# Kernel tuning notes

Measured on AMD Instinct MI355X. Metric: run time of the kernel, lower is better.

## Reference

```python
import jax, jax.numpy as jnp
import numpy as np

B, T, D_MODEL = 4, 4096, 512
HEADS, BUCKET_SIZE, N_HASHES = 8, 64, 4
DIM_HEAD = D_MODEL // HEADS  # 64
D_FFN = 2048
N_BUCKETS = T // BUCKET_SIZE  # 64
SELF_ATTN_VALUE = -5e4  # reformer TOKEN_SELF_ATTN_VALUE


def setup_inputs() -> dict:
    key = jax.random.key(0)
    ks = jax.random.split(key, 16)
    s = 0.02
    return {
        'x': jax.random.normal(ks[0], (B, T, D_MODEL), jnp.float32),
        'rotations': jax.random.normal(ks[1], (DIM_HEAD, N_HASHES, N_BUCKETS // 2), jnp.float32),
        'w_qk': jax.random.normal(ks[2], (D_MODEL, D_MODEL), jnp.float32) * s,
        'w_v': jax.random.normal(ks[3], (D_MODEL, D_MODEL), jnp.float32) * s,
        'w_out': jax.random.normal(ks[4], (D_MODEL, D_MODEL), jnp.float32) * s,
        'b_out': jnp.zeros((D_MODEL,), jnp.float32),
        'ln1_g': jnp.ones((D_MODEL,), jnp.float32),
        'ln1_b': jnp.zeros((D_MODEL,), jnp.float32),
        'w1': jax.random.normal(ks[5], (D_FFN, D_MODEL), jnp.float32) * s,
        'b1': jnp.zeros((D_FFN,), jnp.float32),
        'w2': jax.random.normal(ks[6], (D_MODEL, D_FFN), jnp.float32) * s,
        'b2': jnp.zeros((D_MODEL,), jnp.float32),
        'ln2_g': jnp.ones((D_MODEL,), jnp.float32),
        'ln2_b': jnp.zeros((D_MODEL,), jnp.float32),
    }


def layer_norm(x, g, b, eps=1e-6):
    m = x.mean(-1, keepdims=True)
    v = ((x - m) ** 2).mean(-1, keepdims=True)
    return (x - m) / jnp.sqrt(v + eps) * g + b


def look_one_back(x):
    # concat each chunk with the previous chunk (wrap-around), along in-chunk axis
    prev = jnp.roll(x, 1, axis=1)
    return jnp.concatenate([x, prev], axis=2)


def lsh_attention(qk, v, rotations):
    # qk, v: (bh, t, d) with shared-QK; rotations: (d, n_hashes, n_buckets//2)
    bh, t, d = qk.shape
    # --- hash: random rotations, argmax over [R, -R] ---
    rot = jnp.einsum('btf,fhi->bhti', qk, rotations)
    rot = jnp.concatenate([rot, -rot], axis=-1)        # (bh, H, t, n_buckets)
    buckets = jnp.argmax(rot, axis=-1)                 # (bh, H, t)
    buckets = buckets + (jnp.arange(N_HASHES) * N_BUCKETS)[None, :, None]
    buckets = buckets.reshape(bh, N_HASHES * t)
    # --- sort by (bucket, position) ---
    ticker = jnp.arange(N_HASHES * t)
    buckets_and_t = t * buckets + (ticker % t)[None, :]
    sticker = jnp.argsort(buckets_and_t, axis=-1)      # stable sort
    undo_sort = jnp.argsort(sticker, axis=-1)
    st = sticker % t                                   # original positions, sorted order
    sqk = jnp.take_along_axis(qk, st[..., None], axis=1)
    sv = jnp.take_along_axis(v, st[..., None], axis=1)
    # --- chunk: n_hashes*n_buckets chunks of bucket_size tokens ---
    n_chunks = N_HASHES * N_BUCKETS
    bq_t = st.reshape(bh, n_chunks, -1)
    bqk = sqk.reshape(bh, n_chunks, -1, d)
    bv = sv.reshape(bh, n_chunks, -1, d)
    bk = bqk / jnp.clip(jnp.linalg.norm(bqk, axis=-1, keepdims=True), 1e-6, None)
    bk = look_one_back(bk)
    bv = look_one_back(bv)
    bkv_t = look_one_back(bq_t)
    # --- local attention within chunk (+ previous chunk) ---
    dots = jnp.einsum('bcid,bcjd->bcij', bqk, bk) * (DIM_HEAD ** -0.5)
    self_mask = bq_t[..., None] == bkv_t[..., None, :]
    dots = jnp.where(self_mask, SELF_ATTN_VALUE, dots)
    logits = jax.nn.logsumexp(dots, axis=-1, keepdims=True)
    probs = jnp.exp(dots - logits)
    bo = jnp.einsum('bcij,bcjd->bcid', probs, bv)
    # --- unsort and combine hash rounds by softmax over round logits ---
    so = bo.reshape(bh, N_HASHES * t, d)
    slogits = logits.reshape(bh, N_HASHES * t)
    o = jnp.take_along_axis(so, undo_sort[..., None], axis=1).reshape(bh, N_HASHES, t, d)
    lg = jnp.take_along_axis(slogits, undo_sort, axis=1).reshape(bh, N_HASHES, t, 1)
    w = jnp.exp(lg - jax.nn.logsumexp(lg, axis=1, keepdims=True))
    return (o * w).sum(axis=1)                         # (bh, t, d)


def reference(x, rotations, w_qk, w_v, w_out, b_out, ln1_g, ln1_b, w1, b1, w2, b2, ln2_g, ln2_b):
    b, t, _ = x.shape
    qk = x @ w_qk.T
    v = x @ w_v.T

    def split_heads(u):
        return u.reshape(b, t, HEADS, DIM_HEAD).transpose(0, 2, 1, 3).reshape(b * HEADS, t, DIM_HEAD)

    attn = lsh_attention(split_heads(qk), split_heads(v), rotations)
    attn = attn.reshape(b, HEADS, t, DIM_HEAD).transpose(0, 2, 1, 3).reshape(b, t, D_MODEL)
    attn = attn @ w_out.T + b_out
    # residual + LN (dropout is identity at inference)
    h = layer_norm(attn + x, ln1_g, ln1_b)
    # position-wise FFN with its own residual + LN
    f = jax.nn.relu(h @ w1.T + b1) @ w2.T + b2
    return layer_norm(f + h, ln2_g, ln2_b)
```

## Files before the change

### kernel.cpp

```cpp
#include <hip/hip_runtime.h>
#include <stdint.h>

typedef unsigned short u16;
typedef __attribute__((ext_vector_type(4))) int   i32x4;
typedef __attribute__((ext_vector_type(4))) float f32x4;

__device__ __forceinline__ u16 f2bf(float x){
  unsigned int u = __float_as_uint(x);
  u += 0x7FFFu + ((u >> 16) & 1u);
  return (u16)(u >> 16);
}
__device__ __forceinline__ float bf2f(u16 h){
  return __uint_as_float(((unsigned int)h) << 16);
}
__device__ __forceinline__ f32x4 mfma16(i32x4 a, i32x4 b, f32x4 c){
  asm("v_mfma_f32_16x16x32_bf16 %0, %1, %2, %0" : "+v"(c) : "v"(a), "v"(b));
  return c;
}
__device__ __forceinline__ f32x4 acc_fence(f32x4 c){
  asm volatile("s_nop 7\ns_nop 7" : "+v"(c));
  return c;
}
__device__ __forceinline__ void gl_lds16(const void* g, void* l){
  unsigned long long ga = (unsigned long long)g;
  unsigned int la = (unsigned int)(unsigned long long)l;
  __builtin_amdgcn_global_load_lds((const __attribute__((address_space(1))) void*)ga,
                                   (__attribute__((address_space(3))) void*)la, 16, 0, 0);
}
__device__ __forceinline__ unsigned int f2mono(float v){
  unsigned int u = __float_as_uint(v);
  return u ^ ((unsigned int)((int)u >> 31) | 0x80000000u);
}
__device__ __forceinline__ float mono2f(unsigned int mu){
  unsigned int u = (mu & 0x80000000u) ? (mu ^ 0x80000000u) : ~mu;
  return __uint_as_float(u);
}
__device__ __forceinline__ unsigned long long shfl_xor_u64(unsigned long long x, int m){
  int lo = __shfl_xor((int)(unsigned int)(x & 0xFFFFFFFFull), m);
  int hi = __shfl_xor((int)(unsigned int)(x >> 32), m);
  return ((unsigned long long)(unsigned int)hi << 32) | (unsigned int)lo;
}

__global__ __launch_bounds__(256) void k_cvt(const float* __restrict__ in, u16* __restrict__ out, int n4){
  int i = blockIdx.x*256 + threadIdx.x;
  if (i >= n4) return;
  float4 v = ((const float4*)in)[i];
  ushort4 o; o.x=f2bf(v.x); o.y=f2bf(v.y); o.z=f2bf(v.z); o.w=f2bf(v.w);
  ((ushort4*)out)[i] = o;
}
__global__ __launch_bounds__(256) void k_split(const float* __restrict__ in, u16* __restrict__ hi, u16* __restrict__ lo, int n4){
  int i = blockIdx.x*256 + threadIdx.x;
  if (i >= n4) return;
  float4 v = ((const float4*)in)[i];
  ushort4 h, l;
  h.x=f2bf(v.x); l.x=f2bf(v.x - bf2f(h.x));
  h.y=f2bf(v.y); l.y=f2bf(v.y - bf2f(h.y));
  h.z=f2bf(v.z); l.z=f2bf(v.z - bf2f(h.z));
  h.w=f2bf(v.w); l.w=f2bf(v.w - bf2f(h.w));
  ((ushort4*)hi)[i]=h; ((ushort4*)lo)[i]=l;
}
__global__ __launch_bounds__(256) void k_rotT(const float* __restrict__ rot, u16* __restrict__ hi, u16* __restrict__ lo){
  int i = blockIdx.x*256 + threadIdx.x;
  if (i >= 8192) return;
  int d = i & 63, n = i >> 6;
  float v = rot[d*128 + n];
  u16 h = f2bf(v);
  hi[i] = h; lo[i] = f2bf(v - bf2f(h));
}

template<int MODE>
__global__ __launch_bounds__(256) void k_gemm(
    const u16* __restrict__ A0, const u16* __restrict__ A1,
    const u16* __restrict__ B0, const u16* __restrict__ B1,
    const float* __restrict__ bias,
    float* __restrict__ Cf, u16* __restrict__ Cb,
    int M, int N, int K, int nterms)
{
  const int tid = threadIdx.x;
  const int l = tid & 63, w = tid >> 6;
  const int lr = l & 15, lg = l >> 4;
  const int m0 = blockIdx.y * 128, n0 = blockIdx.x * 128;
  const int mbase = (w >> 1) * 64, nbase = (w & 1) * 64;

  __shared__ __align__(16) u16 As[128*64];
  __shared__ __align__(16) u16 Bs[128*64];

  f32x4 zero = {0.f,0.f,0.f,0.f};
  f32x4 acc[4][4];
  #pragma unroll
  for (int i=0;i<4;i++)
    #pragma unroll
    for (int j=0;j<4;j++) acc[i][j] = zero;

  const int row_s = tid >> 3;
  const int c16   = tid & 7;

  for (int term = 0; term < nterms; ++term){
    const u16* Ap = (term==2) ? A1 : A0;
    const u16* Bp = (term==1) ? B1 : B0;
    for (int k0 = 0; k0 < K; k0 += 64){
      #pragma unroll
      for (int q=0;q<4;q++){
        int ra = q*32 + row_s;
        int cs = c16 ^ (ra & 7);
        gl_lds16(Ap + (size_t)(m0 + ra)*K + k0 + cs*8, (char*)As + q*4096 + tid*16);
        gl_lds16(Bp + (size_t)(n0 + ra)*K + k0 + cs*8, (char*)Bs + q*4096 + tid*16);
      }
      __syncthreads();
      #pragma unroll
      for (int kk=0; kk<64; kk+=32){
        i32x4 af[4], bfr[4];
        #pragma unroll
        for (int mf=0;mf<4;mf++){
          int row = mbase + mf*16 + lr;
          af[mf] = *(const i32x4*)((const char*)As + row*128 + (((kk*2) + (lg*16)) ^ ((row&7)<<4)));
        }
        #pragma unroll
        for (int nf=0;nf<4;nf++){
          int row = nbase + nf*16 + lr;
          bfr[nf] = *(const i32x4*)((const char*)Bs + row*128 + (((kk*2) + (lg*16)) ^ ((row&7)<<4)));
        }
        #pragma unroll
        for (int mf=0;mf<4;mf++)
          #pragma unroll
          for (int nf=0;nf<4;nf++)
            acc[mf][nf] = mfma16(af[mf], bfr[nf], acc[mf][nf]);
      }
      __syncthreads();
    }
  }

  #pragma unroll
  for (int mf=0;mf<4;mf++){
    #pragma unroll
    for (int nf=0;nf<4;nf++){
      f32x4 v = acc_fence(acc[mf][nf]);
      #pragma unroll
      for (int r=0;r<4;r++){
        int m = m0 + mbase + mf*16 + lg*4 + r;
        int n = n0 + nbase + nf*16 + lr;
        float val = v[r];
        if (MODE == 0){
          if (bias) val += bias[n];
          Cf[(size_t)m*N + n] = val;
        } else if (MODE == 1){
          val += bias[n];
          val = fmaxf(val, 0.f);
          Cb[(size_t)m*N + n] = f2bf(val);
        } else {
          int b = m >> 12, t = m & 4095, h = n >> 6, d = n & 63;
          size_t idx = ((((size_t)(b*8 + h)) << 12) + t)*64 + d;
          if (MODE == 2) Cf[idx] = val;
          else           Cb[idx] = f2bf(val);
        }
      }
    }
  }
}

__global__ __launch_bounds__(256) void k_hash2(
    const u16* __restrict__ qh, const u16* __restrict__ ql,
    const u16* __restrict__ rh, const u16* __restrict__ rl,
    int* __restrict__ bkt)
{
  const int tid = threadIdx.x;
  const int l = tid & 63, w = tid >> 6, lr = l & 15, lg = l >> 4;
  __shared__ __align__(16) u16 Rh[128*64];
  __shared__ __align__(16) u16 Rl[128*64];
  {
    const int row_s = tid >> 3, c8 = tid & 7;
    #pragma unroll
    for (int q = 0; q < 4; q++){
      int ra = q*32 + row_s;
      int cs = c8 ^ (ra & 7);
      gl_lds16(rh + ra*64 + cs*8, (char*)Rh + q*4096 + tid*16);
      gl_lds16(rl + ra*64 + cs*8, (char*)Rl + q*4096 + tid*16);
    }
  }
  const int qrow = blockIdx.x*64 + w*16 + lr;
  const size_t qoff = (size_t)qrow*64;
  i32x4 qhf[2], qlf[2];
  qhf[0] = *(const i32x4*)(qh + qoff + lg*8);
  qhf[1] = *(const i32x4*)(qh + qoff + 32 + lg*8);
  qlf[0] = *(const i32x4*)(ql + qoff + lg*8);
  qlf[1] = *(const i32x4*)(ql + qoff + 32 + lg*8);
  __syncthreads();

  f32x4 zero = {0.f,0.f,0.f,0.f};
  f32x4 acc[8];
  #pragma unroll
  for (int i=0;i<8;i++) acc[i] = zero;
  #pragma unroll
  for (int ks = 0; ks < 2; ks++){
    #pragma unroll
    for (int nf = 0; nf < 8; nf++){
      int row = nf*16 + lr;
      int off = (ks*64 + lg*16) ^ ((row & 7) << 4);
      i32x4 rhf = *(const i32x4*)((const char*)Rh + row*128 + off);
      i32x4 rlf = *(const i32x4*)((const char*)Rl + row*128 + off);
      acc[nf] = mfma16(rhf, qhf[ks], acc[nf]);
      acc[nf] = mfma16(rlf, qhf[ks], acc[nf]);
      acc[nf] = mfma16(rhf, qlf[ks], acc[nf]);
    }
  }

  const int bh = qrow >> 12, t = qrow & 4095;
  #pragma unroll
  for (int hh = 0; hh < 4; hh++){
    f32x4 v0 = acc_fence(acc[2*hh]);
    f32x4 v1 = acc_fence(acc[2*hh+1]);
    unsigned long long kmax = 0, kmin = 0;
    #pragma unroll
    for (int r = 0; r < 4; r++){
      int j0 = lg*4 + r, j1 = 16 + lg*4 + r;
      unsigned int mu0 = f2mono(v0[r]), mu1 = f2mono(v1[r]);
      unsigned long long a = ((unsigned long long)mu0 << 32) | (unsigned int)(31 - j0);
      unsigned long long b = ((unsigned long long)mu1 << 32) | (unsigned int)(31 - j1);
      if (a > kmax) kmax = a;
      if (b > kmax) kmax = b;
      unsigned long long c = ((unsigned long long)(~mu0) << 32) | (unsigned int)(31 - j0);
      unsigned long long d = ((unsigned long long)(~mu1) << 32) | (unsigned int)(31 - j1);
      if (c > kmin) kmin = c;
      if (d > kmin) kmin = d;
    }
    #pragma unroll
    for (int msk = 16; msk < 64; msk <<= 1){
      unsigned long long o1 = shfl_xor_u64(kmax, msk); if (o1 > kmax) kmax = o1;
      unsigned long long o2 = shfl_xor_u64(kmin, msk); if (o2 > kmin) kmin = o2;
    }
    if (lg == 0){
      float vmax = mono2f((unsigned int)(kmax >> 32));
      int jmax = 31 - (int)(kmax & 0xFFFFFFFFull);
      float vmin = mono2f(~(unsigned int)(kmin >> 32));
      int jmin = 31 - (int)(kmin & 0xFFFFFFFFull);
      int bucket = (vmax >= -vmin) ? jmax : 32 + jmin;
      bkt[((size_t)(bh*4 + hh) << 12) + t] = bucket;
    }
  }
}

__global__ __launch_bounds__(256) void k_prep(const float* __restrict__ qkf,
                                              u16* __restrict__ qb, u16* __restrict__ qlo,
                                              u16* __restrict__ kn){
  const int row = blockIdx.x*16 + (threadIdx.x >> 4);
  const int l16 = threadIdx.x & 15;
  float4 v = *(const float4*)(qkf + (size_t)row*64 + l16*4);
  float ss = v.x*v.x + v.y*v.y + v.z*v.z + v.w*v.w;
  ss += __shfl_xor(ss, 1); ss += __shfl_xor(ss, 2);
  ss += __shfl_xor(ss, 4); ss += __shfl_xor(ss, 8);
  float scale = 1.f / fmaxf(sqrtf(ss), 1e-6f);
  u16 h0=f2bf(v.x), h1=f2bf(v.y), h2=f2bf(v.z), h3=f2bf(v.w);
  uint q0 = (uint)h0 | ((uint)h1<<16);
  uint q1 = (uint)h2 | ((uint)h3<<16);
  uint e0 = (uint)f2bf(v.x-bf2f(h0)) | ((uint)f2bf(v.y-bf2f(h1))<<16);
  uint e1 = (uint)f2bf(v.z-bf2f(h2)) | ((uint)f2bf(v.w-bf2f(h3))<<16);
  uint k0 = (uint)f2bf(v.x*scale) | ((uint)f2bf(v.y*scale)<<16);
  uint k1 = (uint)f2bf(v.z*scale) | ((uint)f2bf(v.w*scale)<<16);
  uint2 qo = {q0,q1}, eo = {e0,e1}, ko = {k0,k1};
  ((uint2*)(qb  + (size_t)row*64))[l16] = qo;
  ((uint2*)(qlo + (size_t)row*64))[l16] = eo;
  ((uint2*)(kn  + (size_t)row*64))[l16] = ko;
}

__global__ __launch_bounds__(64) void k_sort(const int* __restrict__ buckets, int* __restrict__ st){
  const int grp = blockIdx.x;
  const int t = threadIdx.x;
  __shared__ int hist[64][65];
  __shared__ int tot[64];
  const size_t gbase = ((size_t)grp) << 12;
  #pragma unroll
  for (int b=0;b<64;b++) hist[t][b] = 0;
  __syncthreads();
  for (int i=0;i<64;i++){
    int b = buckets[gbase + t*64 + i];
    hist[t][b]++;
  }
  __syncthreads();
  { int run = 0;
    for (int tt=0; tt<64; tt++){ int v = hist[tt][t]; hist[tt][t] = run; run += v; }
    tot[t] = run; }
  __syncthreads();
  { int v = tot[t]; int incl = v;
    #pragma unroll
    for (int d=1; d<64; d<<=1){ int n = __shfl_up(incl, d, 64); if (t >= d) incl += n; }
    tot[t] = incl - v; }
  __syncthreads();
  const size_t obase = (((size_t)(grp>>2)) << 14) + ((size_t)(grp&3) << 12);
  for (int i=0;i<64;i++){
    int e = t*64 + i;
    int b = buckets[gbase + e];
    int dest = tot[b] + hist[t][b];
    hist[t][b]++;
    st[obase + dest] = e;
  }
}

__global__ __launch_bounds__(256, 4) void k_attn(
    const u16* __restrict__ qb, const u16* __restrict__ kn, const u16* __restrict__ vB,
    const int* __restrict__ st, float* __restrict__ lgt_out, u16* __restrict__ bo)
{
  const int c = blockIdx.x, bh = blockIdx.y;
  const int rnd = c >> 6;
  const int tid = threadIdx.x;
  const int l = tid & 63, w = tid >> 6, lr = l & 15, lg = l >> 4;

  __shared__ __align__(16) u16 Ks[128*64];
  __shared__ __align__(16) u16 Vt[64][136];
  __shared__ int posk[128];

  if (tid < 128){
    int cc = (tid < 64) ? c : ((c + 255) & 255);
    posk[tid] = st[(((size_t)bh) << 14) + (cc << 6) + (tid & 63)];
  }
  __syncthreads();

  const size_t kvbase = ((size_t)bh) << 12;

  {
    const int rsub = l >> 3, c8 = l & 7;
    #pragma unroll
    for (int q2 = 0; q2 < 4; q2++){
      int row = w*32 + q2*8 + rsub;
      int cs = c8 ^ (row & 7);
      gl_lds16(kn + (kvbase + posk[row])*64 + cs*8,
               (char*)Ks + (w*4 + q2)*1024 + l*16);
    }
  }

  const int pos_q16 = posk[w*16 + lr];
  i32x4 qf[2];
  #pragma unroll
  for (int ks = 0; ks < 2; ks++)
    qf[ks] = *(const i32x4*)(qb + (kvbase + pos_q16)*64 + ks*32 + lg*8);

  {
    const int pp = tid & 63, db = tid >> 6;
    const int q5 = pp & 15;
    const int K0 = (pp >> 4)*32 + 16*((q5 >> 1) & 1) + 4*(q5 >> 2) + 2*(q5 & 1);
    const u16* r0 = vB + (kvbase + posk[K0])*64 + db*16;
    const u16* r1 = vB + (kvbase + posk[K0+1])*64 + db*16;
    uint4 a0 = *(const uint4*)r0, a1 = *(const uint4*)(r0 + 8);
    uint4 b0 = *(const uint4*)r1, b1 = *(const uint4*)(r1 + 8);
    uint av[8] = {a0.x,a0.y,a0.z,a0.w,a1.x,a1.y,a1.z,a1.w};
    uint bv[8] = {b0.x,b0.y,b0.z,b0.w,b1.x,b1.y,b1.z,b1.w};
    #pragma unroll
    for (int dd = 0; dd < 16; dd++){
      uint lo = (av[dd>>1] >> ((dd&1)*16)) & 0xFFFFu;
      uint hi = (bv[dd>>1] >> ((dd&1)*16)) & 0xFFFFu;
      *(uint*)((char*)&Vt[db*16 + dd][0] + pp*4) = lo | (hi << 16);
    }
  }
  __syncthreads();

  f32x4 zero = {0.f,0.f,0.f,0.f};
  f32x4 s[8];
  #pragma unroll
  for (int i=0;i<8;i++) s[i] = zero;
  #pragma unroll
  for (int ks = 0; ks < 2; ks++){
    #pragma unroll
    for (int nf = 0; nf < 8; nf++){
      int row = nf*16 + lr;
      i32x4 kf = *(const i32x4*)((const char*)Ks + row*128 + ((ks*64 + lg*16) ^ ((row&7)<<4)));
      s[nf] = mfma16(kf, qf[ks], s[nf]);
    }
  }

  float sv[8][4];
  const int q_loc = w*16 + lr;
  #pragma unroll
  for (int nf=0;nf<8;nf++){
    f32x4 t = acc_fence(s[nf]);
    #pragma unroll
    for (int r=0;r<4;r++){
      int k = nf*16 + lg*4 + r;
      sv[nf][r] = (k == q_loc) ? -5e4f : t[r]*0.125f;
    }
  }
  float m = -1e30f;
  #pragma unroll
  for (int nf=0;nf<8;nf++)
    #pragma unroll
    for (int r=0;r<4;r++) m = fmaxf(m, sv[nf][r]);
  m = fmaxf(m, __shfl_xor(m, 16));
  m = fmaxf(m, __shfl_xor(m, 32));
  float sum = 0.f;
  #pragma unroll
  for (int nf=0;nf<8;nf++)
    #pragma unroll
    for (int r=0;r<4;r++) sum += __expf(sv[nf][r] - m);
  sum += __shfl_xor(sum, 16);
  sum += __shfl_xor(sum, 32);
  float lv = m + logf(sum);
  if (l < 16)
    lgt_out[(((size_t)(bh*4 + rnd)) << 12) + pos_q16] = lv;

  i32x4 pa[4];
  #pragma unroll
  for (int ks=0;ks<4;ks++){
    uint wd[4];
    #pragma unroll
    for (int h2=0; h2<2; h2++){
      int nf = 2*ks + h2;
      float p0 = __expf(sv[nf][0]-lv), p1 = __expf(sv[nf][1]-lv);
      float p2 = __expf(sv[nf][2]-lv), p3 = __expf(sv[nf][3]-lv);
      wd[h2*2]   = (uint)f2bf(p0) | ((uint)f2bf(p1)<<16);
      wd[h2*2+1] = (uint)f2bf(p2) | ((uint)f2bf(p3)<<16);
    }
    i32x4 t = {(int)wd[0],(int)wd[1],(int)wd[2],(int)wd[3]};
    pa[ks] = t;
  }

  f32x4 o[4];
  #pragma unroll
  for (int i=0;i<4;i++) o[i] = zero;
  #pragma unroll
  for (int ks=0;ks<4;ks++){
    #pragma unroll
    for (int nf=0;nf<4;nf++){
      i32x4 vf = *(const i32x4*)((const char*)&Vt[nf*16 + lr][0] + ks*64 + lg*16);
      o[nf] = mfma16(pa[ks], vf, o[nf]);
    }
  }
  #pragma unroll
  for (int nf=0;nf<4;nf++){
    f32x4 ov = acc_fence(o[nf]);
    #pragma unroll
    for (int r=0;r<4;r++){
      int q = w*16 + lg*4 + r;
      bo[((((size_t)(bh*4 + rnd)) << 12) + posk[q])*64 + nf*16 + lr] = f2bf(ov[r]);
    }
  }
}

__global__ __launch_bounds__(256) void k_combine(const u16* __restrict__ bo, const float* __restrict__ lgt,
                                                 u16* __restrict__ attn){
  const int wid = blockIdx.x * 4 + (threadIdx.x >> 6);
  const int l = threadIdx.x & 63;
  const int bh = wid >> 12, t = wid & 4095;
  const size_t lbase = (((size_t)bh) << 14) + t;
  float l0 = lgt[lbase], l1 = lgt[lbase + 4096], l2 = lgt[lbase + 8192], l3 = lgt[lbase + 12288];
  float m = fmaxf(fmaxf(l0,l1), fmaxf(l2,l3));
  float w0 = __expf(l0-m), w1 = __expf(l1-m), w2 = __expf(l2-m), w3 = __expf(l3-m);
  float inv = 1.f / (w0+w1+w2+w3);
  const size_t bbase = ((((size_t)bh) << 14) + t) * 64 + l;
  float o = w0 * bf2f(bo[bbase])
          + w1 * bf2f(bo[bbase + (size_t)4096*64])
          + w2 * bf2f(bo[bbase + (size_t)8192*64])
          + w3 * bf2f(bo[bbase + (size_t)12288*64]);
  o *= inv;
  int b = bh >> 3, h = bh & 7;
  attn[((((size_t)b) << 12) + t) * 512 + h*64 + l] = f2bf(o);
}

template<int WB16>
__global__ __launch_bounds__(256) void k_ln(const float* __restrict__ a, const float* __restrict__ res,
                                            const float* __restrict__ g, const float* __restrict__ bb,
                                            float* __restrict__ of, u16* __restrict__ ob){
  const int row = blockIdx.x*4 + (threadIdx.x >> 6);
  const int l = threadIdx.x & 63;
  const size_t base = (size_t)row*512 + l*8;
  float4 a0 = *(const float4*)(a + base);
  float4 a1 = *(const float4*)(a + base + 4);
  float4 r0 = *(const float4*)(res + base);
  float4 r1 = *(const float4*)(res + base + 4);
  float v[8] = {a0.x+r0.x, a0.y+r0.y, a0.z+r0.z, a0.w+r0.w,
                a1.x+r1.x, a1.y+r1.y, a1.z+r1.z, a1.w+r1.w};
  float sum = 0.f;
  #pragma unroll
  for (int j=0;j<8;j++) sum += v[j];
  #pragma unroll
  for (int msk=1; msk<64; msk<<=1) sum += __shfl_xor(sum, msk);
  float mean = sum * (1.f/512.f);
  float ss = 0.f;
  #pragma unroll
  for (int j=0;j<8;j++){ float d = v[j]-mean; ss += d*d; }
  #pragma unroll
  for (int msk=1; msk<64; msk<<=1) ss += __shfl_xor(ss, msk);
  float rstd = rsqrtf(ss * (1.f/512.f) + 1e-6f);
  float4 g0 = *(const float4*)(g + l*8),  g1 = *(const float4*)(g + l*8 + 4);
  float4 b0 = *(const float4*)(bb + l*8), b1 = *(const float4*)(bb + l*8 + 4);
  float gv[8] = {g0.x,g0.y,g0.z,g0.w,g1.x,g1.y,g1.z,g1.w};
  float bv[8] = {b0.x,b0.y,b0.z,b0.w,b1.x,b1.y,b1.z,b1.w};
  float y[8];
  #pragma unroll
  for (int j=0;j<8;j++) y[j] = (v[j]-mean)*rstd*gv[j] + bv[j];
  #pragma unroll
  for (int j=0;j<8;j++) of[base+j] = y[j];
  if (WB16){
    #pragma unroll
    for (int j=0;j<8;j++) ob[base+j] = f2bf(y[j]);
  }
}

extern "C" void kernel_launch(void* const* d_in, const int* in_sizes, int n_in,
                              void* d_out, int out_size, void* d_ws, size_t ws_size,
                              hipStream_t stream) {
  const float* x     = (const float*)d_in[0];
  const float* rot   = (const float*)d_in[1];
  const float* w_qk  = (const float*)d_in[2];
  const float* w_v   = (const float*)d_in[3];
  const float* w_out = (const float*)d_in[4];
  const float* b_out = (const float*)d_in[5];
  const float* ln1_g = (const float*)d_in[6];
  const float* ln1_b = (const float*)d_in[7];
  const float* w1    = (const float*)d_in[8];
  const float* b1    = (const float*)d_in[9];
  const float* w2    = (const float*)d_in[10];
  const float* b2    = (const float*)d_in[11];
  const float* ln2_g = (const float*)d_in[12];
  const float* ln2_b = (const float*)d_in[13];
  float* out = (float*)d_out;

  char* p = (char*)d_ws;
  u16*   xh   = (u16*)(p);
  u16*   xl   = (u16*)(p + 16777216);
  u16*   wqkh = (u16*)(p + 33554432);
  u16*   wqkl = (u16*)(p + 34078720);
  u16*   wvb  = (u16*)(p + 34603008);
  u16*   wob  = (u16*)(p + 35127296);
  u16*   w1b  = (u16*)(p + 35651584);
  u16*   w2b  = (u16*)(p + 37748736);
  float* qkf  = (float*)(p + 39845888);
  u16*   vb   = (u16*)(p + 73400320);
  int*   bkt  = (int*)(p + 90177536);
  int*   stb  = (int*)(p + 92274688);
  float* lgt  = (float*)(p + 94371840);
  u16*   bo   = (u16*)(p + 96468992);
  u16*   qbuf  = xh;
  u16*   knb   = xl;
  u16*   qlo   = bo;
  u16*   rothi = wqkh;
  u16*   rotlo = wqkl;
  u16*   attnc = xl;
  float* hf    = qkf;
  u16*   hb    = xh;
  u16*   hid   = bo;

  k_split<<<8192, 256, 0, stream>>>(x, xh, xl, 16384*512/4);
  k_split<<<256,  256, 0, stream>>>(w_qk, wqkh, wqkl, 512*512/4);
  k_cvt  <<<256,  256, 0, stream>>>(w_v,   wvb, 512*512/4);
  k_cvt  <<<256,  256, 0, stream>>>(w_out, wob, 512*512/4);
  k_cvt  <<<1024, 256, 0, stream>>>(w1, w1b, 2048*512/4);
  k_cvt  <<<1024, 256, 0, stream>>>(w2, w2b, 2048*512/4);

  k_gemm<2><<<dim3(4,128), 256, 0, stream>>>(xh, xl, wqkh, wqkl, nullptr, qkf, nullptr, 16384, 512, 512, 3);
  k_gemm<3><<<dim3(4,128), 256, 0, stream>>>(xh, nullptr, wvb, nullptr, nullptr, nullptr, vb, 16384, 512, 512, 1);
  k_rotT<<<32, 256, 0, stream>>>(rot, rothi, rotlo);
  k_prep<<<8192, 256, 0, stream>>>(qkf, qbuf, qlo, knb);
  k_hash2<<<2048, 256, 0, stream>>>(qbuf, qlo, rothi, rotlo, bkt);
  k_sort<<<128, 64, 0, stream>>>(bkt, stb);
  k_attn<<<dim3(256,32), 256, 0, stream>>>(qbuf, knb, vb, stb, lgt, bo);
  k_combine<<<32768, 256, 0, stream>>>(bo, lgt, attnc);
  k_gemm<0><<<dim3(4,128), 256, 0, stream>>>(attnc, nullptr, wob, nullptr, b_out, out, nullptr, 16384, 512, 512, 1);
  k_ln<1><<<4096, 256, 0, stream>>>(out, x, ln1_g, ln1_b, hf, hb);
  k_gemm<1><<<dim3(16,128), 256, 0, stream>>>(hb, nullptr, w1b, nullptr, b1, nullptr, hid, 16384, 2048, 512, 1);
  k_gemm<0><<<dim3(4,128), 256, 0, stream>>>(hid, nullptr, w2b, nullptr, b2, out, nullptr, 16384, 512, 2048, 1);
  k_ln<0><<<4096, 256, 0, stream>>>(out, hf, ln2_g, ln2_b, out, nullptr);
}
```

Measured before the change: 352.2 us.

## Fuse QK prep into GEMM epilogue, add XCD block swizzle, reuse softmax exps

The QK projection GEMM now writes the bf16 hi/lo split and the L2-normalized key directly from its epilogue, using a row-norm shuffle reduction. This removes the k_prep kernel and the fp32 qk round trip through memory. Block indices in the GEMM, hash and attention kernels are remapped so neighbouring tiles land on the same XCD, aiming for better L2 reuse. The attention softmax keeps the exponentials and multiplies by a reciprocal instead of recomputing exp. The workspace layout changes so qbuf and knb no longer alias xh and xl, which the QK GEMM still reads.

```diff
diff --git a/kernel.cpp b/kernel.cpp
--- a/kernel.cpp
+++ b/kernel.cpp
@@ -26,6 +26,10 @@
   unsigned int la = (unsigned int)(unsigned long long)l;
   __builtin_amdgcn_global_load_lds((const __attribute__((address_space(1))) void*)ga,
                                    (__attribute__((address_space(3))) void*)la, 16, 0, 0);
+}
+__device__ __forceinline__ int xcd_swz(int f, int n){
+  int chunk = n >> 3;
+  return (f & 7) * chunk + (f >> 3);
 }
 __device__ __forceinline__ unsigned int f2mono(float v){
   unsigned int u = __float_as_uint(v);
@@ -74,12 +78,15 @@
     const u16* __restrict__ B0, const u16* __restrict__ B1,
     const float* __restrict__ bias,
     float* __restrict__ Cf, u16* __restrict__ Cb,
+    u16* __restrict__ Cb2, u16* __restrict__ Cb3,
     int M, int N, int K, int nterms)
 {
   const int tid = threadIdx.x;
   const int l = tid & 63, w = tid >> 6;
   const int lr = l & 15, lg = l >> 4;
-  const int m0 = blockIdx.y * 128, n0 = blockIdx.x * 128;
+  int flat = blockIdx.y * gridDim.x + blockIdx.x;
+  flat = xcd_swz(flat, gridDim.x * gridDim.y);
+  const int m0 = (flat / gridDim.x) * 128, n0 = (flat % gridDim.x) * 128;
   const int mbase = (w >> 1) * 64, nbase = (w & 1) * 64;
 
   __shared__ __align__(16) u16 As[128*64];
@@ -130,6 +137,38 @@
     }
   }
 
+  if (MODE == 2){
+    const int hh = (n0 + nbase) >> 6;
+    #pragma unroll
+    for (int mf=0;mf<4;mf++){
+      f32x4 v[4];
+      #pragma unroll
+      for (int nf=0;nf<4;nf++) v[nf] = acc_fence(acc[mf][nf]);
+      #pragma unroll
+      for (int r=0;r<4;r++){
+        float ss = 0.f;
+        #pragma unroll
+        for (int nf=0;nf<4;nf++) ss += v[nf][r]*v[nf][r];
+        ss += __shfl_xor(ss, 1); ss += __shfl_xor(ss, 2);
+        ss += __shfl_xor(ss, 4); ss += __shfl_xor(ss, 8);
+        float scale = 1.f / fmaxf(sqrtf(ss), 1e-6f);
+        int m = m0 + mbase + mf*16 + lg*4 + r;
+        int b = m >> 12, t = m & 4095;
+        size_t rowb = ((((size_t)(b*8 + hh)) << 12) + t) * 64;
+        #pragma unroll
+        for (int nf=0;nf<4;nf++){
+          float val = v[nf][r];
+          u16 hbf = f2bf(val);
+          size_t idx = rowb + nf*16 + lr;
+          Cb [idx] = hbf;
+          Cb2[idx] = f2bf(val - bf2f(hbf));
+          Cb3[idx] = f2bf(val * scale);
+        }
+      }
+    }
+    return;
+  }
+
   #pragma unroll
   for (int mf=0;mf<4;mf++){
     #pragma unroll
@@ -150,8 +189,7 @@
         } else {
           int b = m >> 12, t = m & 4095, h = n >> 6, d = n & 63;
           size_t idx = ((((size_t)(b*8 + h)) << 12) + t)*64 + d;
-          if (MODE == 2) Cf[idx] = val;
-          else           Cb[idx] = f2bf(val);
+          Cb[idx] = f2bf(val);
         }
       }
     }
@@ -177,7 +215,8 @@
       gl_lds16(rl + ra*64 + cs*8, (char*)Rl + q*4096 + tid*16);
     }
   }
-  const int qrow = blockIdx.x*64 + w*16 + lr;
+  const int blk = xcd_swz(blockIdx.x, gridDim.x);
+  const int qrow = blk*64 + w*16 + lr;
   const size_t qoff = (size_t)qrow*64;
   i32x4 qhf[2], qlf[2];
   qhf[0] = *(const i32x4*)(qh + qoff + lg*8);
@@ -239,29 +278,6 @@
   }
 }
 
-__global__ __launch_bounds__(256) void k_prep(const float* __restrict__ qkf,
-                                              u16* __restrict__ qb, u16* __restrict__ qlo,
-                                              u16* __restrict__ kn){
-  const int row = blockIdx.x*16 + (threadIdx.x >> 4);
-  const int l16 = threadIdx.x & 15;
-  float4 v = *(const float4*)(qkf + (size_t)row*64 + l16*4);
-  float ss = v.x*v.x + v.y*v.y + v.z*v.z + v.w*v.w;
-  ss += __shfl_xor(ss, 1); ss += __shfl_xor(ss, 2);
-  ss += __shfl_xor(ss, 4); ss += __shfl_xor(ss, 8);
-  float scale = 1.f / fmaxf(sqrtf(ss), 1e-6f);
-  u16 h0=f2bf(v.x), h1=f2bf(v.y), h2=f2bf(v.z), h3=f2bf(v.w);
-  uint q0 = (uint)h0 | ((uint)h1<<16);
-  uint q1 = (uint)h2 | ((uint)h3<<16);
-  uint e0 = (uint)f2bf(v.x-bf2f(h0)) | ((uint)f2bf(v.y-bf2f(h1))<<16);
-  uint e1 = (uint)f2bf(v.z-bf2f(h2)) | ((uint)f2bf(v.w-bf2f(h3))<<16);
-  uint k0 = (uint)f2bf(v.x*scale) | ((uint)f2bf(v.y*scale)<<16);
-  uint k1 = (uint)f2bf(v.z*scale) | ((uint)f2bf(v.w*scale)<<16);
-  uint2 qo = {q0,q1}, eo = {e0,e1}, ko = {k0,k1};
-  ((uint2*)(qb  + (size_t)row*64))[l16] = qo;
-  ((uint2*)(qlo + (size_t)row*64))[l16] = eo;
-  ((uint2*)(kn  + (size_t)row*64))[l16] = ko;
-}
-
 __global__ __launch_bounds__(64) void k_sort(const int* __restrict__ buckets, int* __restrict__ st){
   const int grp = blockIdx.x;
   const int t = threadIdx.x;
@@ -299,7 +315,9 @@
     const u16* __restrict__ qb, const u16* __restrict__ kn, const u16* __restrict__ vB,
     const int* __restrict__ st, float* __restrict__ lgt_out, u16* __restrict__ bo)
 {
-  const int c = blockIdx.x, bh = blockIdx.y;
+  int flat = blockIdx.y * gridDim.x + blockIdx.x;
+  flat = xcd_swz(flat, gridDim.x * gridDim.y);
+  const int c = flat & 255, bh = flat >> 8;
   const int rnd = c >> 6;
   const int tid = threadIdx.x;
   const int l = tid & 63, w = tid >> 6, lr = l & 15, lg = l >> 4;
@@ -388,10 +406,11 @@
   #pragma unroll
   for (int nf=0;nf<8;nf++)
     #pragma unroll
-    for (int r=0;r<4;r++) sum += __expf(sv[nf][r] - m);
+    for (int r=0;r<4;r++){ sv[nf][r] = __expf(sv[nf][r] - m); sum += sv[nf][r]; }
   sum += __shfl_xor(sum, 16);
   sum += __shfl_xor(sum, 32);
   float lv = m + logf(sum);
+  float inv = 1.f / sum;
   if (l < 16)
     lgt_out[(((size_t)(bh*4 + rnd)) << 12) + pos_q16] = lv;
 
@@ -402,8 +421,8 @@
     #pragma unroll
     for (int h2=0; h2<2; h2++){
       int nf = 2*ks + h2;
-      float p0 = __expf(sv[nf][0]-lv), p1 = __expf(sv[nf][1]-lv);
-      float p2 = __expf(sv[nf][2]-lv), p3 = __expf(sv[nf][3]-lv);
+      float p0 = sv[nf][0]*inv, p1 = sv[nf][1]*inv;
+      float p2 = sv[nf][2]*inv, p3 = sv[nf][3]*inv;
       wd[h2*2]   = (uint)f2bf(p0) | ((uint)f2bf(p1)<<16);
       wd[h2*2+1] = (uint)f2bf(p2) | ((uint)f2bf(p3)<<16);
     }
@@ -521,19 +540,18 @@
   u16*   wob  = (u16*)(p + 35127296);
   u16*   w1b  = (u16*)(p + 35651584);
   u16*   w2b  = (u16*)(p + 37748736);
-  float* qkf  = (float*)(p + 39845888);
+  u16*   qbuf = (u16*)(p + 39845888);
+  u16*   knb  = (u16*)(p + 56623104);
   u16*   vb   = (u16*)(p + 73400320);
   int*   bkt  = (int*)(p + 90177536);
   int*   stb  = (int*)(p + 92274688);
   float* lgt  = (float*)(p + 94371840);
   u16*   bo   = (u16*)(p + 96468992);
-  u16*   qbuf  = xh;
-  u16*   knb   = xl;
   u16*   qlo   = bo;
   u16*   rothi = wqkh;
   u16*   rotlo = wqkl;
   u16*   attnc = xl;
-  float* hf    = qkf;
+  float* hf    = (float*)(p + 39845888);
   u16*   hb    = xh;
   u16*   hid   = bo;
 
@@ -544,17 +562,16 @@
   k_cvt  <<<1024, 256, 0, stream>>>(w1, w1b, 2048*512/4);
   k_cvt  <<<1024, 256, 0, stream>>>(w2, w2b, 2048*512/4);
 
-  k_gemm<2><<<dim3(4,128), 256, 0, stream>>>(xh, xl, wqkh, wqkl, nullptr, qkf, nullptr, 16384, 512, 512, 3);
-  k_gemm<3><<<dim3(4,128), 256, 0, stream>>>(xh, nullptr, wvb, nullptr, nullptr, nullptr, vb, 16384, 512, 512, 1);
+  k_gemm<2><<<dim3(4,128), 256, 0, stream>>>(xh, xl, wqkh, wqkl, nullptr, nullptr, qbuf, qlo, knb, 16384, 512, 512, 3);
+  k_gemm<3><<<dim3(4,128), 256, 0, stream>>>(xh, nullptr, wvb, nullptr, nullptr, nullptr, vb, nullptr, nullptr, 16384, 512, 512, 1);
   k_rotT<<<32, 256, 0, stream>>>(rot, rothi, rotlo);
-  k_prep<<<8192, 256, 0, stream>>>(qkf, qbuf, qlo, knb);
   k_hash2<<<2048, 256, 0, stream>>>(qbuf, qlo, rothi, rotlo, bkt);
   k_sort<<<128, 64, 0, stream>>>(bkt, stb);
   k_attn<<<dim3(256,32), 256, 0, stream>>>(qbuf, knb, vb, stb, lgt, bo);
   k_combine<<<32768, 256, 0, stream>>>(bo, lgt, attnc);
-  k_gemm<0><<<dim3(4,128), 256, 0, stream>>>(attnc, nullptr, wob, nullptr, b_out, out, nullptr, 16384, 512, 512, 1);
+  k_gemm<0><<<dim3(4,128), 256, 0, stream>>>(attnc, nullptr, wob, nullptr, b_out, out, nullptr, nullptr, nullptr, 16384, 512, 512, 1);
   k_ln<1><<<4096, 256, 0, stream>>>(out, x, ln1_g, ln1_b, hf, hb);
-  k_gemm<1><<<dim3(16,128), 256, 0, stream>>>(hb, nullptr, w1b, nullptr, b1, nullptr, hid, 16384, 2048, 512, 1);
-  k_gemm<0><<<dim3(4,128), 256, 0, stream>>>(hid, nullptr, w2b, nullptr, b2, out, nullptr, 16384, 512, 2048, 1);
+  k_gemm<1><<<dim3(16,128), 256, 0, stream>>>(hb, nullptr, w1b, nullptr, b1, nullptr, hid, nullptr, nullptr, 16384, 2048, 512, 1);
+  k_gemm<0><<<dim3(4,128), 256, 0, stream>>>(hid, nullptr, w2b, nullptr, b2, out, nullptr, nullptr, nullptr, 16384, 512, 2048, 1);
   k_ln<0><<<4096, 256, 0, stream>>>(out, hf, ln2_g, ln2_b, out, nullptr);
 }
```

New measurement: 333.9 us. 5.2% less time.
